# Performance work log

Hardware: AMD Instinct MI355X
Metric: run time of the kernel (lower is better)

Reference implementation:

```python
import jax, jax.numpy as jnp
import numpy as np
from jax import lax


def _conv2d(x, w, b, stride):
    # x: [B,C,H,W], w: [O,I,kh,kw], b: [O]
    y = lax.conv_general_dilated(
        x, w, window_strides=(stride, stride), padding='VALID',
        dimension_numbers=('NCHW', 'OIHW', 'NCHW'))
    return y + b[None, :, None, None]


def setup_inputs() -> dict:
    key = jax.random.key(0)
    ks = jax.random.split(key, 4)
    B, C, H, W = 8, 128, 128, 128
    x = jax.random.normal(ks[0], (B, C, H, W), dtype=jnp.float32)
    # conv weights, scaled like torch default init (~1/sqrt(fan_in))
    Wq = jax.random.normal(ks[1], (C, C, 2, 2), dtype=jnp.float32) / np.sqrt(C * 4)
    Wk = jax.random.normal(ks[2], (C, C, 2, 2), dtype=jnp.float32) / np.sqrt(C * 4)
    Wv = jax.random.normal(ks[3], (C, C, 1, 1), dtype=jnp.float32) / np.sqrt(C)
    bq = jnp.zeros((C,), dtype=jnp.float32)
    bk = jnp.zeros((C,), dtype=jnp.float32)
    bv = jnp.zeros((C,), dtype=jnp.float32)
    return {'x': x, 'Wq': Wq, 'bq': bq, 'Wk': Wk, 'bk': bk, 'Wv': Wv, 'bv': bv}


def reference(x, Wq, bq, Wk, bk, Wv, bv):
    B, C, H, W = x.shape
    # query/key: 2x2 stride-2 convs -> [B, C, (H//2)*(W//2)]
    q = _conv2d(x, Wq, bq, 2).reshape(B, C, -1)
    k = _conv2d(x, Wk, bk, 2).reshape(B, C, -1)
    # value: 1x1 conv -> [B, C, H*W]
    v = _conv2d(x, Wv, bv, 1).reshape(B, C, -1)
    # energy: [B, C, C]
    energy = jnp.einsum('bcn,bdn->bcd', q, k)
    # max-subtract trick: softmax over (row_max - energy)
    energy_new = jnp.max(energy, axis=-1, keepdims=True) - energy
    attention = jax.nn.softmax(energy_new, axis=-1)
    out = jnp.einsum('bcd,bdn->bcn', attention, v)
    return out.reshape(B, C, H, W)
```

## Files before the change

kernel.cpp:

```cpp
#include <hip/hip_runtime.h>
#include <math.h>


typedef float f32x4 __attribute__((ext_vector_type(4)));
typedef short s16x8 __attribute__((ext_vector_type(8)));

__device__ __forceinline__ unsigned short f2bf(float f) {
  union { __bf16 b; unsigned short u; } v;
  v.b = (__bf16)f;
  return v.u;
}
__device__ __forceinline__ float bf2f(unsigned short h) {
  union { unsigned u; float f; } v; v.u = ((unsigned)h) << 16;
  return v.f;
}
__device__ __forceinline__ unsigned pack2(unsigned short a, unsigned short b) {
  return (unsigned)a | ((unsigned)b << 16);
}

__global__ __launch_bounds__(256) void k_prep(
    const float* __restrict__ Wq, const float* __restrict__ Wk,
    unsigned short* __restrict__ Wth, unsigned short* __restrict__ Wtl) {
  const int f = (blockIdx.x * 256 + threadIdx.x) * 4;
  const int row = f >> 9;
  const int k   = f & 511;
  const float* src = (row < 128) ? &Wq[row * 512 + k] : &Wk[(row - 128) * 512 + k];
  float4 v = *(const float4*)src;
  unsigned short h0 = f2bf(v.x), h1 = f2bf(v.y), h2 = f2bf(v.z), h3 = f2bf(v.w);
  unsigned short l0 = f2bf(v.x - bf2f(h0)), l1 = f2bf(v.y - bf2f(h1));
  unsigned short l2 = f2bf(v.z - bf2f(h2)), l3 = f2bf(v.w - bf2f(h3));
  const int di = (k >> 5) * 8192 + row * 32 + (k & 31);
  *(ushort4*)&Wth[di] = make_ushort4(h0, h1, h2, h3);
  *(ushort4*)&Wtl[di] = make_ushort4(l0, l1, l2, l3);
}

__global__ __launch_bounds__(512) void k_conv_energy(
    const float* __restrict__ x,
    const unsigned short* __restrict__ Wth, const unsigned short* __restrict__ Wtl,
    const float* __restrict__ bq, const float* __restrict__ bk,
    float* __restrict__ epart) {
  __shared__ unsigned short LDS[20480];
  unsigned short* Th = LDS;
  unsigned short* Tl = LDS + 8192;

  const int t = threadIdx.x;
  const int nt = blockIdx.x, b = blockIdx.y;
  const int w = t >> 6, lane = t & 63;
  const int wr = w >> 1, wc = w & 1;
  const int lrow = lane & 15, lkb = lane >> 4;

  const int ci_l = t >> 6;
  const int kh = (t >> 5) & 1;
  const int i32 = t & 31;
  const int klb = ci_l * 4 + kh * 2;
  const float* xb = x + ((size_t)b << 21);
  const float* xrow = xb + (size_t)ci_l * 16384 + (4 * nt + kh) * 128 + 2 * i32;

  f32x4 acc[4][4];
#pragma unroll
  for (int m = 0; m < 4; ++m)
#pragma unroll
    for (int n = 0; n < 4; ++n) acc[m][n] = (f32x4){0.f, 0.f, 0.f, 0.f};

  s16x8 pfh[4], pfl[4];
  float2 pv[2][4];
  const int aoff = (wr * 64 + lrow) * 32 + lkb * 8;
  const int goff[4] = {0, 64, 256, 320};

#pragma unroll
  for (int m = 0; m < 4; ++m) {
    pfh[m] = *(const s16x8*)&Wth[aoff + m * 512];
    pfl[m] = *(const s16x8*)&Wtl[aoff + m * 512];
  }
#pragma unroll
  for (int g = 0; g < 4; ++g) {
    float2 v = *(const float2*)&xrow[goff[g]];
    const int col = i32 + 32 * g;
    unsigned short hx = f2bf(v.x), hy = f2bf(v.y);
    *(unsigned*)&LDS[col * 40 + klb] = pack2(hx, hy);
    *(unsigned*)&LDS[5120 + col * 40 + klb] =
        pack2(f2bf(v.x - bf2f(hx)), f2bf(v.y - bf2f(hy)));
  }
#pragma unroll
  for (int g = 0; g < 4; ++g)
    pv[1][g] = *(const float2*)&xrow[(size_t)8 * 16384 + goff[g]];
  __syncthreads();

#pragma unroll
  for (int step = 0; step < 16; ++step) {
    const int cur = step & 1;
    const unsigned short* Bh = LDS + cur * 10240;
    const unsigned short* Bl = Bh + 5120;
    s16x8 bfh[4], bfl[4];
#pragma unroll
    for (int nf = 0; nf < 4; ++nf) {
      const int bidx = (wc * 64 + nf * 16 + lrow) * 40 + lkb * 8;
      bfh[nf] = *(const s16x8*)&Bh[bidx];
      bfl[nf] = *(const s16x8*)&Bl[bidx];
    }
#pragma unroll
    for (int m = 0; m < 4; ++m)
#pragma unroll
      for (int n = 0; n < 4; ++n) {
        acc[m][n] = __builtin_amdgcn_mfma_f32_16x16x32_bf16(pfh[m], bfh[n], acc[m][n], 0, 0, 0);
        acc[m][n] = __builtin_amdgcn_mfma_f32_16x16x32_bf16(pfh[m], bfl[n], acc[m][n], 0, 0, 0);
        acc[m][n] = __builtin_amdgcn_mfma_f32_16x16x32_bf16(pfl[m], bfh[n], acc[m][n], 0, 0, 0);
      }
    if (step < 15) {
      const unsigned short* Wh_n = Wth + (step + 1) * 8192;
      const unsigned short* Wl_n = Wtl + (step + 1) * 8192;
#pragma unroll
      for (int m = 0; m < 4; ++m) {
        pfh[m] = *(const s16x8*)&Wh_n[aoff + m * 512];
        pfl[m] = *(const s16x8*)&Wl_n[aoff + m * 512];
      }
    }
    if (step < 14) {
#pragma unroll
      for (int g = 0; g < 4; ++g)
        pv[cur][g] = *(const float2*)&xrow[(size_t)(step + 2) * 8 * 16384 + goff[g]];
    }
    if (step < 15) {
      unsigned short* Nh = LDS + (cur ^ 1) * 10240;
      unsigned short* Nl = Nh + 5120;
#pragma unroll
      for (int g = 0; g < 4; ++g) {
        const int col = i32 + 32 * g;
        unsigned short hx = f2bf(pv[cur ^ 1][g].x), hy = f2bf(pv[cur ^ 1][g].y);
        *(unsigned*)&Nh[col * 40 + klb] = pack2(hx, hy);
        *(unsigned*)&Nl[col * 40 + klb] = pack2(f2bf(pv[cur ^ 1][g].x - bf2f(hx)),
                                                f2bf(pv[cur ^ 1][g].y - bf2f(hy)));
      }
      asm volatile("s_waitcnt lgkmcnt(0)" ::: "memory");
      __builtin_amdgcn_s_barrier();
    }
  }
  __syncthreads();

  const float* biasp = (wr < 2) ? bq : bk;
  const int rb = (wr & 1) * 64;
  float biasr[16];
#pragma unroll
  for (int m = 0; m < 4; ++m)
#pragma unroll
    for (int i = 0; i < 4; ++i)
      biasr[m * 4 + i] = biasp[rb + m * 16 + (lane >> 4) * 4 + i];

  f32x4 e[2][4];
#pragma unroll
  for (int mm = 0; mm < 2; ++mm)
#pragma unroll
    for (int nf = 0; nf < 4; ++nf) e[mm][nf] = (f32x4){0.f, 0.f, 0.f, 0.f};

  const int qg = w >> 1;
  const int kg = w & 1;

#pragma unroll
  for (int ks = 0; ks < 4; ++ks) {
    if (wc == (ks >> 1)) {
#pragma unroll
      for (int m = 0; m < 4; ++m) {
        const int r0 = wr * 64 + m * 16 + (lane >> 4) * 4;
#pragma unroll
        for (int nn = 0; nn < 2; ++nn) {
          const int n = 2 * (ks & 1) + nn;
          const int cl = nn * 16 + lrow;
          const int cl8 = cl >> 3, c7 = cl & 7;
#pragma unroll
          for (int i = 0; i < 4; ++i) {
            const int r = r0 + i;
            const float vv = acc[m][n][i] + biasr[m * 4 + i];
            const unsigned short h = f2bf(vv);
            const unsigned short l = f2bf(vv - bf2f(h));
            const int ad = r * 32 + ((cl8 ^ (r & 3)) << 3) + c7;
            Th[ad] = h;
            Tl[ad] = l;
          }
        }
      }
    }
    __syncthreads();
    {
      s16x8 qh[2], ql[2], kh8[4], kl8[4];
#pragma unroll
      for (int mm = 0; mm < 2; ++mm) {
        const int r = qg * 32 + mm * 16 + lrow;
        const int ad = r * 32 + ((lkb ^ (r & 3)) << 3);
        qh[mm] = *(const s16x8*)&Th[ad];
        ql[mm] = *(const s16x8*)&Tl[ad];
      }
#pragma unroll
      for (int nf = 0; nf < 4; ++nf) {
        const int r = 128 + kg * 64 + nf * 16 + lrow;
        const int ad = r * 32 + ((lkb ^ (r & 3)) << 3);
        kh8[nf] = *(const s16x8*)&Th[ad];
        kl8[nf] = *(const s16x8*)&Tl[ad];
      }
#pragma unroll
      for (int mm = 0; mm < 2; ++mm)
#pragma unroll
        for (int nf = 0; nf < 4; ++nf) {
          e[mm][nf] = __builtin_amdgcn_mfma_f32_16x16x32_bf16(qh[mm], kh8[nf], e[mm][nf], 0, 0, 0);
          e[mm][nf] = __builtin_amdgcn_mfma_f32_16x16x32_bf16(qh[mm], kl8[nf], e[mm][nf], 0, 0, 0);
          e[mm][nf] = __builtin_amdgcn_mfma_f32_16x16x32_bf16(ql[mm], kh8[nf], e[mm][nf], 0, 0, 0);
        }
    }
    if (ks < 3) __syncthreads();
  }

  float* ep = epart + ((size_t)b * 32 + nt) * 16384;
#pragma unroll
  for (int mm = 0; mm < 2; ++mm) {
    const int qr0 = qg * 32 + mm * 16 + (lane >> 4) * 4;
#pragma unroll
    for (int nf = 0; nf < 4; ++nf) {
      const int kc = kg * 64 + nf * 16 + (lane & 15);
#pragma unroll
      for (int i = 0; i < 4; ++i)
        ep[(size_t)(qr0 + i) * 128 + kc] = e[mm][nf][i];
    }
  }
}

__global__ __launch_bounds__(256) void k_softmax_M(
    const float* __restrict__ epart, const float* __restrict__ Wv,
    const float* __restrict__ bv, float* __restrict__ Mbuf,
    float* __restrict__ outbb) {
  __shared__ float As[4][128];
  const int t = threadIdx.x;
  const int wid = t >> 6, lane = t & 63;
  const int b = blockIdx.x >> 5;
  const int c = (blockIdx.x & 31) * 4 + wid;
  const int d0 = lane * 2;

  float2 s = make_float2(0.f, 0.f);
#pragma unroll 4
  for (int p = 0; p < 32; ++p) {
    float2 e = *(const float2*)&epart[((size_t)b * 32 + p) * 16384 + c * 128 + d0];
    s.x += e.x; s.y += e.y;
  }
  float mn = fminf(s.x, s.y);
#pragma unroll
  for (int off = 1; off < 64; off <<= 1) mn = fminf(mn, __shfl_xor(mn, off));
  const float p0 = expf(mn - s.x);
  const float p1 = expf(mn - s.y);
  float tot = p0 + p1;
#pragma unroll
  for (int off = 1; off < 64; off <<= 1) tot += __shfl_xor(tot, off);
  const float inv = 1.f / tot;
  const float a0 = p0 * inv, a1 = p1 * inv;

  const float2 bvv = *(const float2*)&bv[d0];
  float ob = a0 * bvv.x + a1 * bvv.y;
#pragma unroll
  for (int off = 1; off < 64; off <<= 1) ob += __shfl_xor(ob, off);
  if (lane == 0) outbb[b * 128 + c] = ob;

  As[wid][d0] = a0;
  As[wid][d0 + 1] = a1;
  float m0 = 0.f, m1 = 0.f;
#pragma unroll 4
  for (int d = 0; d < 128; ++d) {
    const float a = As[wid][d];
    const float2 wv = *(const float2*)&Wv[d * 128 + d0];
    m0 = fmaf(a, wv.x, m0);
    m1 = fmaf(a, wv.y, m1);
  }
  *(float2*)&Mbuf[(size_t)b * 16384 + c * 128 + d0] = make_float2(m0, m1);
}

__global__ __launch_bounds__(256) void k_out(
    const float* __restrict__ x, const float* __restrict__ Mbuf,
    const float* __restrict__ outbb, float* __restrict__ out) {
  __shared__ unsigned short Ms[128 * 40];
  __shared__ unsigned short Xs[128 * 40];
  const int t = threadIdx.x;
  const int nt = blockIdx.x, b = blockIdx.y;
  const int wid = t >> 6, lane = t & 63;
  const int wr = wid >> 1, wc = wid & 1;
  const int lrow = lane & 15, lkb = lane >> 4;
  const int am = t >> 1, ak0 = (t & 1) * 16;
  const int xkl = (t >> 5) * 4;
  const int xc0 = (t & 31) * 4;

  const float* xb = x + ((size_t)b << 21);
  const float* Mb = Mbuf + (size_t)b * 16384;
  float* ob = out + ((size_t)b << 21);

  f32x4 acc[4][4];
#pragma unroll
  for (int m = 0; m < 4; ++m)
#pragma unroll
    for (int n = 0; n < 4; ++n) acc[m][n] = (f32x4){0.f, 0.f, 0.f, 0.f};

  for (int step = 0; step < 4; ++step) {
    const int kk = step * 32;
    {
      float w[16];
      *(float4*)&w[0]  = *(const float4*)&Mb[am * 128 + kk + ak0];
      *(float4*)&w[4]  = *(const float4*)&Mb[am * 128 + kk + ak0 + 4];
      *(float4*)&w[8]  = *(const float4*)&Mb[am * 128 + kk + ak0 + 8];
      *(float4*)&w[12] = *(const float4*)&Mb[am * 128 + kk + ak0 + 12];
      unsigned short hs[16];
#pragma unroll
      for (int i = 0; i < 16; ++i) hs[i] = f2bf(w[i]);
      *(uint4*)&Ms[am * 40 + ak0]     = *(uint4*)&hs[0];
      *(uint4*)&Ms[am * 40 + ak0 + 8] = *(uint4*)&hs[8];
    }
#pragma unroll
    for (int q = 0; q < 4; ++q) {
      const int kl = xkl + q;
      float4 v = *(const float4*)&xb[(size_t)(kk + kl) * 16384 + nt * 128 + xc0];
      Xs[(xc0 + 0) * 40 + kl] = f2bf(v.x);
      Xs[(xc0 + 1) * 40 + kl] = f2bf(v.y);
      Xs[(xc0 + 2) * 40 + kl] = f2bf(v.z);
      Xs[(xc0 + 3) * 40 + kl] = f2bf(v.w);
    }
    __syncthreads();
    s16x8 af[4], bf[4];
#pragma unroll
    for (int m = 0; m < 4; ++m)
      af[m] = *(const s16x8*)&Ms[(wr * 64 + m * 16 + lrow) * 40 + lkb * 8];
#pragma unroll
    for (int n = 0; n < 4; ++n)
      bf[n] = *(const s16x8*)&Xs[(wc * 64 + n * 16 + lrow) * 40 + lkb * 8];
#pragma unroll
    for (int m = 0; m < 4; ++m)
#pragma unroll
      for (int n = 0; n < 4; ++n)
        acc[m][n] = __builtin_amdgcn_mfma_f32_16x16x32_bf16(af[m], bf[n], acc[m][n], 0, 0, 0);
    __syncthreads();
  }
#pragma unroll
  for (int m = 0; m < 4; ++m) {
    const int r0 = wr * 64 + m * 16 + (lane >> 4) * 4;
#pragma unroll
    for (int n = 0; n < 4; ++n) {
      const int gc = nt * 128 + wc * 64 + n * 16 + (lane & 15);
#pragma unroll
      for (int i = 0; i < 4; ++i) {
        const int row = r0 + i;
        ob[(size_t)row * 16384 + gc] = acc[m][n][i] + outbb[b * 128 + row];
      }
    }
  }
}

extern "C" void kernel_launch(void* const* d_in, const int* in_sizes, int n_in,
                              void* d_out, int out_size, void* d_ws, size_t ws_size,
                              hipStream_t stream) {
  const float* x  = (const float*)d_in[0];
  const float* Wq = (const float*)d_in[1];
  const float* bq = (const float*)d_in[2];
  const float* Wk = (const float*)d_in[3];
  const float* bk = (const float*)d_in[4];
  const float* Wv = (const float*)d_in[5];
  const float* bv = (const float*)d_in[6];
  float* out = (float*)d_out;
  char* ws = (char*)d_ws;

  float* epart = (float*)ws;
  float* Mbuf  = (float*)(ws + 16777216);
  float* outbb = (float*)(ws + 17301504);
  unsigned short* Wth = (unsigned short*)(ws + 17305600);
  unsigned short* Wtl = (unsigned short*)(ws + 17567744);

  hipLaunchKernelGGL(k_prep, dim3(128), dim3(256), 0, stream, Wq, Wk, Wth, Wtl);
  hipLaunchKernelGGL(k_conv_energy, dim3(32, 8), dim3(512), 0, stream,
                     x, Wth, Wtl, bq, bk, epart);
  hipLaunchKernelGGL(k_softmax_M, dim3(256), dim3(256), 0, stream,
                     epart, Wv, bv, Mbuf, outbb);
  hipLaunchKernelGGL(k_out, dim3(128, 8), dim3(256), 0, stream,
                     x, Mbuf, outbb, out);
}
```

Before: 81.66 us.

## Switch conv GEMM to 32x32x16 MFMA with vectorized LDS staging

Replaces the 16x16x32 bf16 MFMA tiling of the q/k conv GEMM with 32x32x16 MFMA tiles (2x2 per wave). The input-staging thread mapping changes so each thread writes a single 16-byte hi/lo vector to LDS instead of four 4-byte stores. Weight fragments are now loaded from global inside each step rather than prefetched one step ahead. The epilogue is remapped to the 32x32 accumulator layout. The goal is fewer MFMA issues and fewer LDS store instructions, at the cost of losing the weight prefetch, which may expose global load latency.

```diff
diff --git a/kernel.cpp b/kernel.cpp
--- a/kernel.cpp
+++ b/kernel.cpp
@@ -2,8 +2,9 @@
 #include <math.h>
 
 
-typedef float f32x4 __attribute__((ext_vector_type(4)));
-typedef short s16x8 __attribute__((ext_vector_type(8)));
+typedef float f32x4  __attribute__((ext_vector_type(4)));
+typedef float f32x16 __attribute__((ext_vector_type(16)));
+typedef short s16x8  __attribute__((ext_vector_type(8)));
 
 __device__ __forceinline__ unsigned short f2bf(float f) {
   union { __bf16 b; unsigned short u; } v;
@@ -16,6 +17,12 @@
 }
 __device__ __forceinline__ unsigned pack2(unsigned short a, unsigned short b) {
   return (unsigned)a | ((unsigned)b << 16);
+}
+__device__ __forceinline__ void cvt_hilo(float a, float b,
+                                         unsigned& hw, unsigned& lw) {
+  unsigned short ha = f2bf(a), hb = f2bf(b);
+  hw = pack2(ha, hb);
+  lw = pack2(f2bf(a - bf2f(ha)), f2bf(b - bf2f(hb)));
 }
 
 __global__ __launch_bounds__(256) void k_prep(
@@ -47,43 +54,46 @@
   const int nt = blockIdx.x, b = blockIdx.y;
   const int w = t >> 6, lane = t & 63;
   const int wr = w >> 1, wc = w & 1;
-  const int lrow = lane & 15, lkb = lane >> 4;
-
-  const int ci_l = t >> 6;
-  const int kh = (t >> 5) & 1;
-  const int i32 = t & 31;
-  const int klb = ci_l * 4 + kh * 2;
+  const int l31 = lane & 31, l5 = lane >> 5;
+
+  const int col_s = t & 127;
+  const int kseg  = t >> 7;
+  const int ci0   = 2 * kseg;
+  const int ohl   = col_s >> 6;
+  const int ow    = col_s & 63;
   const float* xb = x + ((size_t)b << 21);
-  const float* xrow = xb + (size_t)ci_l * 16384 + (4 * nt + kh) * 128 + 2 * i32;
-
-  f32x4 acc[4][4];
-#pragma unroll
-  for (int m = 0; m < 4; ++m)
-#pragma unroll
-    for (int n = 0; n < 4; ++n) acc[m][n] = (f32x4){0.f, 0.f, 0.f, 0.f};
-
-  s16x8 pfh[4], pfl[4];
+  const float* xs = xb + (size_t)ci0 * 16384 + (nt * 4 + ohl * 2) * 128 + 2 * ow;
+  const int sidx = col_s * 40 + kseg * 8;
+
+  f32x16 acc[2][2];
+#pragma unroll
+  for (int tm = 0; tm < 2; ++tm)
+#pragma unroll
+    for (int tn = 0; tn < 2; ++tn)
+#pragma unroll
+      for (int r = 0; r < 16; ++r) acc[tm][tn][r] = 0.f;
+
   float2 pv[2][4];
-  const int aoff = (wr * 64 + lrow) * 32 + lkb * 8;
-  const int goff[4] = {0, 64, 256, 320};
-
-#pragma unroll
-  for (int m = 0; m < 4; ++m) {
-    pfh[m] = *(const s16x8*)&Wth[aoff + m * 512];
-    pfl[m] = *(const s16x8*)&Wtl[aoff + m * 512];
-  }
-#pragma unroll
-  for (int g = 0; g < 4; ++g) {
-    float2 v = *(const float2*)&xrow[goff[g]];
-    const int col = i32 + 32 * g;
-    unsigned short hx = f2bf(v.x), hy = f2bf(v.y);
-    *(unsigned*)&LDS[col * 40 + klb] = pack2(hx, hy);
-    *(unsigned*)&LDS[5120 + col * 40 + klb] =
-        pack2(f2bf(v.x - bf2f(hx)), f2bf(v.y - bf2f(hy)));
-  }
-#pragma unroll
-  for (int g = 0; g < 4; ++g)
-    pv[1][g] = *(const float2*)&xrow[(size_t)8 * 16384 + goff[g]];
+  const int aoff0 = (wr * 64 + l31) * 32 + l5 * 8;
+  const int boff0 = (wc * 64 + l31) * 40 + l5 * 8;
+
+  {
+    float2 p0 = *(const float2*)&xs[0];
+    float2 p1 = *(const float2*)&xs[128];
+    float2 p2 = *(const float2*)&xs[16384];
+    float2 p3 = *(const float2*)&xs[16384 + 128];
+    uint4 hi, lo;
+    cvt_hilo(p0.x, p0.y, hi.x, lo.x);
+    cvt_hilo(p1.x, p1.y, hi.y, lo.y);
+    cvt_hilo(p2.x, p2.y, hi.z, lo.z);
+    cvt_hilo(p3.x, p3.y, hi.w, lo.w);
+    *(uint4*)&LDS[sidx]        = hi;
+    *(uint4*)&LDS[5120 + sidx] = lo;
+  }
+  pv[1][0] = *(const float2*)&xs[(size_t)8 * 16384];
+  pv[1][1] = *(const float2*)&xs[(size_t)8 * 16384 + 128];
+  pv[1][2] = *(const float2*)&xs[(size_t)8 * 16384 + 16384];
+  pv[1][3] = *(const float2*)&xs[(size_t)8 * 16384 + 16384 + 128];
   __syncthreads();
 
 #pragma unroll
@@ -91,46 +101,53 @@
     const int cur = step & 1;
     const unsigned short* Bh = LDS + cur * 10240;
     const unsigned short* Bl = Bh + 5120;
-    s16x8 bfh[4], bfl[4];
-#pragma unroll
-    for (int nf = 0; nf < 4; ++nf) {
-      const int bidx = (wc * 64 + nf * 16 + lrow) * 40 + lkb * 8;
-      bfh[nf] = *(const s16x8*)&Bh[bidx];
-      bfl[nf] = *(const s16x8*)&Bl[bidx];
-    }
-#pragma unroll
-    for (int m = 0; m < 4; ++m)
-#pragma unroll
-      for (int n = 0; n < 4; ++n) {
-        acc[m][n] = __builtin_amdgcn_mfma_f32_16x16x32_bf16(pfh[m], bfh[n], acc[m][n], 0, 0, 0);
-        acc[m][n] = __builtin_amdgcn_mfma_f32_16x16x32_bf16(pfh[m], bfl[n], acc[m][n], 0, 0, 0);
-        acc[m][n] = __builtin_amdgcn_mfma_f32_16x16x32_bf16(pfl[m], bfh[n], acc[m][n], 0, 0, 0);
-      }
-    if (step < 15) {
-      const unsigned short* Wh_n = Wth + (step + 1) * 8192;
-      const unsigned short* Wl_n = Wtl + (step + 1) * 8192;
-#pragma unroll
-      for (int m = 0; m < 4; ++m) {
-        pfh[m] = *(const s16x8*)&Wh_n[aoff + m * 512];
-        pfl[m] = *(const s16x8*)&Wl_n[aoff + m * 512];
-      }
-    }
+    s16x8 bh[2][2], bl[2][2];
+#pragma unroll
+    for (int tn = 0; tn < 2; ++tn)
+#pragma unroll
+      for (int h = 0; h < 2; ++h) {
+        const int bidx = boff0 + tn * 1280 + h * 16;
+        bh[tn][h] = *(const s16x8*)&Bh[bidx];
+        bl[tn][h] = *(const s16x8*)&Bl[bidx];
+      }
+    const unsigned short* Wh_s = Wth + step * 8192;
+    const unsigned short* Wl_s = Wtl + step * 8192;
+    s16x8 ah[2][2], al[2][2];
+#pragma unroll
+    for (int tm = 0; tm < 2; ++tm)
+#pragma unroll
+      for (int h = 0; h < 2; ++h) {
+        const int aidx = aoff0 + tm * 1024 + h * 16;
+        ah[tm][h] = *(const s16x8*)&Wh_s[aidx];
+        al[tm][h] = *(const s16x8*)&Wl_s[aidx];
+      }
     if (step < 14) {
-#pragma unroll
-      for (int g = 0; g < 4; ++g)
-        pv[cur][g] = *(const float2*)&xrow[(size_t)(step + 2) * 8 * 16384 + goff[g]];
-    }
+      const float* xn = xs + (size_t)(step + 2) * 8 * 16384;
+      pv[cur][0] = *(const float2*)&xn[0];
+      pv[cur][1] = *(const float2*)&xn[128];
+      pv[cur][2] = *(const float2*)&xn[16384];
+      pv[cur][3] = *(const float2*)&xn[16384 + 128];
+    }
+#pragma unroll
+    for (int h = 0; h < 2; ++h)
+#pragma unroll
+      for (int tm = 0; tm < 2; ++tm)
+#pragma unroll
+        for (int tn = 0; tn < 2; ++tn) {
+          acc[tm][tn] = __builtin_amdgcn_mfma_f32_32x32x16_bf16(ah[tm][h], bh[tn][h], acc[tm][tn], 0, 0, 0);
+          acc[tm][tn] = __builtin_amdgcn_mfma_f32_32x32x16_bf16(ah[tm][h], bl[tn][h], acc[tm][tn], 0, 0, 0);
+          acc[tm][tn] = __builtin_amdgcn_mfma_f32_32x32x16_bf16(al[tm][h], bh[tn][h], acc[tm][tn], 0, 0, 0);
+        }
     if (step < 15) {
       unsigned short* Nh = LDS + (cur ^ 1) * 10240;
       unsigned short* Nl = Nh + 5120;
-#pragma unroll
-      for (int g = 0; g < 4; ++g) {
-        const int col = i32 + 32 * g;
-        unsigned short hx = f2bf(pv[cur ^ 1][g].x), hy = f2bf(pv[cur ^ 1][g].y);
-        *(unsigned*)&Nh[col * 40 + klb] = pack2(hx, hy);
-        *(unsigned*)&Nl[col * 40 + klb] = pack2(f2bf(pv[cur ^ 1][g].x - bf2f(hx)),
-                                                f2bf(pv[cur ^ 1][g].y - bf2f(hy)));
-      }
+      uint4 hi, lo;
+      cvt_hilo(pv[cur ^ 1][0].x, pv[cur ^ 1][0].y, hi.x, lo.x);
+      cvt_hilo(pv[cur ^ 1][1].x, pv[cur ^ 1][1].y, hi.y, lo.y);
+      cvt_hilo(pv[cur ^ 1][2].x, pv[cur ^ 1][2].y, hi.z, lo.z);
+      cvt_hilo(pv[cur ^ 1][3].x, pv[cur ^ 1][3].y, hi.w, lo.w);
+      *(uint4*)&Nh[sidx] = hi;
+      *(uint4*)&Nl[sidx] = lo;
       asm volatile("s_waitcnt lgkmcnt(0)" ::: "memory");
       __builtin_amdgcn_s_barrier();
     }
@@ -138,13 +155,13 @@
   __syncthreads();
 
   const float* biasp = (wr < 2) ? bq : bk;
-  const int rb = (wr & 1) * 64;
-  float biasr[16];
-#pragma unroll
-  for (int m = 0; m < 4; ++m)
-#pragma unroll
-    for (int i = 0; i < 4; ++i)
-      biasr[m * 4 + i] = biasp[rb + m * 16 + (lane >> 4) * 4 + i];
+  const int rbase = (wr & 1) * 64;
+  float4 bg[2][4];
+#pragma unroll
+  for (int tm = 0; tm < 2; ++tm)
+#pragma unroll
+    for (int g = 0; g < 4; ++g)
+      bg[tm][g] = *(const float4*)&biasp[rbase + tm * 32 + g * 8 + 4 * l5];
 
   f32x4 e[2][4];
 #pragma unroll
@@ -152,32 +169,26 @@
 #pragma unroll
     for (int nf = 0; nf < 4; ++nf) e[mm][nf] = (f32x4){0.f, 0.f, 0.f, 0.f};
 
+  const int lrow = lane & 15, lkb = lane >> 4;
   const int qg = w >> 1;
   const int kg = w & 1;
 
 #pragma unroll
   for (int ks = 0; ks < 4; ++ks) {
     if (wc == (ks >> 1)) {
-#pragma unroll
-      for (int m = 0; m < 4; ++m) {
-        const int r0 = wr * 64 + m * 16 + (lane >> 4) * 4;
-#pragma unroll
-        for (int nn = 0; nn < 2; ++nn) {
-          const int n = 2 * (ks & 1) + nn;
-          const int cl = nn * 16 + lrow;
-          const int cl8 = cl >> 3, c7 = cl & 7;
-#pragma unroll
-          for (int i = 0; i < 4; ++i) {
-            const int r = r0 + i;
-            const float vv = acc[m][n][i] + biasr[m * 4 + i];
-            const unsigned short h = f2bf(vv);
-            const unsigned short l = f2bf(vv - bf2f(h));
-            const int ad = r * 32 + ((cl8 ^ (r & 3)) << 3) + c7;
-            Th[ad] = h;
-            Tl[ad] = l;
-          }
+      const int tn = ks & 1;
+#pragma unroll
+      for (int tm = 0; tm < 2; ++tm)
+#pragma unroll
+        for (int r = 0; r < 16; ++r) {
+          const int row = wr * 64 + tm * 32 + (r & 3) + 8 * (r >> 2) + 4 * l5;
+          const float vv = acc[tm][tn][r] + ((const float*)&bg[tm][r >> 2])[r & 3];
+          const unsigned short h = f2bf(vv);
+          const unsigned short l = f2bf(vv - bf2f(h));
+          const int ad = row * 32 + (((l31 >> 3) ^ (row & 3)) << 3) + (l31 & 7);
+          Th[ad] = h;
+          Tl[ad] = l;
         }
-      }
     }
     __syncthreads();
     {
```

New measurement: 92.50 us. 1.13x slower.
